# Kernel tuning notes

Measured on AMD Instinct MI355X. Metric: run time of the kernel, lower is better.

Reference implementation:

```python
import jax, jax.numpy as jnp
import numpy as np

N_EMBD = 768

def setup_inputs() -> dict:
    key = jax.random.key(0)
    k1, k2, k3, k4 = jax.random.split(key, 4)
    B, T, head_size = 16, 1024, 128
    x = jax.random.normal(k1, (B, T, N_EMBD), dtype=jnp.float32)
    # nn.Linear(in, out, bias=False): weight stored as (out, in); we store transposed (in, out)
    s = 1.0 / np.sqrt(N_EMBD)
    Wk = jax.random.uniform(k2, (N_EMBD, head_size), jnp.float32, -s, s)
    Wq = jax.random.uniform(k3, (N_EMBD, head_size), jnp.float32, -s, s)
    Wv = jax.random.uniform(k4, (N_EMBD, head_size), jnp.float32, -s, s)
    return {"x": x, "Wk": Wk, "Wq": Wq, "Wv": Wv}

def reference(x, Wk, Wq, Wv):
    B, T, C = x.shape  # C == n_embd == 768
    k = jnp.einsum('btc,ch->bth', x, Wk)
    q = jnp.einsum('btc,ch->bth', x, Wq)
    v = jnp.einsum('btc,ch->bth', x, Wv)
    # NOTE: original scales by C**-0.5 with C = n_embd (768), not head_size.
    wei = jnp.einsum('bth,bsh->bts', q, k) * (C ** -0.5)  # (B, T, T)
    causal = jnp.tril(jnp.ones((T, T), dtype=bool))
    wei = jnp.where(causal, wei, -jnp.inf)
    wei = jax.nn.softmax(wei, axis=-1)
    # dropout p=0.0 -> identity
    return jnp.einsum('bts,bsh->bth', wei, v)
```

## Files before the change

### kernel.cpp

```cpp
#include <hip/hip_runtime.h>
#include <math.h>

#define NTOK   16384
#define NEMBD  768
#define HDIM   128

typedef __attribute__((ext_vector_type(8)))  short short8;
typedef __attribute__((ext_vector_type(16))) float floatx16;

#define MFMA32(a,b,c) __builtin_amdgcn_mfma_f32_32x32x16_bf16(a,b,c,0,0,0)

__device__ __forceinline__ unsigned short f2bf(float f) {
    unsigned u = __float_as_uint(f);
    u += 0x7fff + ((u >> 16) & 1);
    return (unsigned short)(u >> 16);
}
__device__ __forceinline__ unsigned pack2(float a, float b) {
    unsigned r;
    asm("v_cvt_pk_bf16_f32 %0, %1, %2" : "=v"(r) : "v"(a), "v"(b));
    return r;
}
__device__ __forceinline__ unsigned pack2_trunc(float a, float b) {
    return __builtin_amdgcn_perm(__float_as_uint(b), __float_as_uint(a),
                                 0x07060302u);
}
__device__ __forceinline__ void gl_lds16(const void* gptr, void* lptr) {
    __builtin_amdgcn_global_load_lds(
        (const __attribute__((address_space(1))) unsigned int*)gptr,
        (__attribute__((address_space(3))) unsigned int*)lptr, 16, 0, 0);
}

__global__ __launch_bounds__(256) void prep_w(
    const float* __restrict__ Wk, const float* __restrict__ Wq,
    const float* __restrict__ Wv, unsigned short* __restrict__ wt)
{
    __shared__ float T[64 * 65];

    const int tid = threadIdx.x;
    const int bw  = blockIdx.x / 24;
    const int rem = blockIdx.x % 24;
    const int ct  = rem >> 1, dh = rem & 1;
    const int c0  = ct * 64, d0 = dh * 64;
    const float* W = (bw == 0) ? Wk : ((bw == 1) ? Wq : Wv);
    const float scale = (bw == 1)
        ? (0.03608439182435161f * 1.4426950408889634f) : 1.0f;

    #pragma unroll
    for (int pass = 0; pass < 4; ++pass) {
        int idx = pass * 256 + tid;
        int c  = idx >> 4;
        int d4 = idx & 15;
        float4 v = ((const float4*)W)[(size_t)(c0 + c) * 32 + dh * 16 + d4];
        v.x *= scale; v.y *= scale; v.z *= scale; v.w *= scale;
        T[(d4 * 4 + 0) * 65 + c] = v.x;
        T[(d4 * 4 + 1) * 65 + c] = v.y;
        T[(d4 * 4 + 2) * 65 + c] = v.z;
        T[(d4 * 4 + 3) * 65 + c] = v.w;
    }
    __syncthreads();

    #pragma unroll
    for (int pass = 0; pass < 2; ++pass) {
        int idx = pass * 256 + tid;
        int d  = idx >> 3;
        int c8 = idx & 7;
        const float* row = &T[d * 65 + c8 * 8];
        uint4 u = make_uint4(pack2(row[0], row[1]), pack2(row[2], row[3]),
                             pack2(row[4], row[5]), pack2(row[6], row[7]));
        *(uint4*)&wt[(size_t)bw * (HDIM * NEMBD) + (size_t)(d0 + d) * NEMBD
                     + c0 + c8 * 8] = u;
    }
}

__global__ __launch_bounds__(256) void qkv_fused(
    const float* __restrict__ x, const unsigned short* __restrict__ wt,
    unsigned short* __restrict__ kb, unsigned short* __restrict__ qb,
    unsigned short* __restrict__ vT)
{
    __shared__ __align__(16) char As[8192];
    __shared__ __align__(16) char Bs[24576];

    const int tid = threadIdx.x, w = tid >> 6, lane = tid & 63;
    const int l31 = lane & 31, h = lane >> 5;
    const int r8 = lane >> 3, c8 = lane & 7;
    const int wm = w >> 1, wn = w & 1;
    const int bid = blockIdx.x;
    const int b2  = ((bid & 7) << 6) | (bid >> 3);
    const int mtile = b2 >> 1, nh = b2 & 1;
    const int m0 = mtile * 64;
    const int nbase = nh * 192;
    const int arow = tid >> 2, ac = tid & 3;

    floatx16 acc[3];
    #pragma unroll
    for (int j = 0; j < 3; ++j)
        #pragma unroll
        for (int i = 0; i < 16; ++i) acc[j][i] = 0.f;

    const float* asrc = x + (size_t)(m0 + arow) * NEMBD + ac * 16;
    float4 a0 = ((const float4*)asrc)[0];
    float4 a1 = ((const float4*)asrc)[1];
    float4 a2 = ((const float4*)asrc)[2];
    float4 a3 = ((const float4*)asrc)[3];

    for (int it = 0; it < 12; ++it) {
        const int k0 = it * 64;
        __syncthreads();
        #pragma unroll
        for (int j = 0; j < 6; ++j) {
            int rowb = w * 48 + j * 8;
            int row  = rowb + r8;
            gl_lds16((const char*)wt + ((size_t)(nbase + row) * NEMBD + k0) * 2
                         + ((c8 ^ (row & 7)) * 16),
                     Bs + rowb * 128);
        }
        {
            uint4 u0 = make_uint4(pack2(a0.x, a0.y), pack2(a0.z, a0.w),
                                  pack2(a1.x, a1.y), pack2(a1.z, a1.w));
            uint4 u1 = make_uint4(pack2(a2.x, a2.y), pack2(a2.z, a2.w),
                                  pack2(a3.x, a3.y), pack2(a3.z, a3.w));
            int cA = 2 * ac, cB = 2 * ac + 1;
            *(uint4*)(As + arow * 128 + ((cA ^ (arow & 7)) * 16)) = u0;
            *(uint4*)(As + arow * 128 + ((cB ^ (arow & 7)) * 16)) = u1;
        }
        if (it < 11) {
            const float4* src = (const float4*)(asrc + (it + 1) * 64);
            a0 = src[0]; a1 = src[1]; a2 = src[2]; a3 = src[3];
        }
        __syncthreads();
        #pragma unroll
        for (int ks = 0; ks < 4; ++ks) {
            int ar = wm * 32 + l31;
            short8 af = *(const short8*)(As + ar * 128
                                         + (((2*ks + h) ^ (ar & 7)) * 16));
            #pragma unroll
            for (int j = 0; j < 3; ++j) {
                int br = wn * 96 + j * 32 + l31;
                short8 bf = *(const short8*)(Bs + br * 128
                                             + (((2*ks + h) ^ (br & 7)) * 16));
                acc[j] = MFMA32(af, bf, acc[j]);
            }
        }
    }

    const int tbase = m0 + wm * 32;
    #pragma unroll
    for (int j = 0; j < 3; ++j) {
        int n0 = nbase + wn * 96 + j * 32;
        if (n0 < 256) {
            unsigned short* outp = (n0 < 128) ? kb : qb;
            int d = (n0 & 127) + l31;
            #pragma unroll
            for (int r = 0; r < 16; ++r) {
                int t = tbase + (r & 3) + 8 * (r >> 2) + 4 * h;
                outp[(size_t)t * HDIM + d] = f2bf(acc[j][r]);
            }
        } else {
            int d = (n0 - 256) + l31, b = m0 >> 10, tloc = (m0 & 1023) + wm * 32;
            #pragma unroll
            for (int g = 0; g < 4; ++g) {
                int t = tloc + 8 * g + 4 * h;
                uint2 u = make_uint2(pack2(acc[j][4*g+0], acc[j][4*g+1]),
                                     pack2(acc[j][4*g+2], acc[j][4*g+3]));
                *(uint2*)((char*)vT + (((size_t)(b * HDIM + d)) * 1024 + t) * 2) = u;
            }
        }
    }
}

__global__ __launch_bounds__(256) void attn_mfma(
    const unsigned short* __restrict__ qb, const unsigned short* __restrict__ kb,
    const unsigned short* __restrict__ vT, float* __restrict__ out)
{
    __shared__ __align__(16) float Obuf[4 * 32 * 128];
    __shared__ float lred[128];

    const int tid = threadIdx.x, w = tid >> 6, lane = tid & 63;
    const int l31 = lane & 31, h = lane >> 5;
    const int u  = blockIdx.x & 255;
    const int b  = u & 15, p = u >> 4;
    const int qt = (blockIdx.x >> 8) ? (31 - p) : p;

    const char* kb_b = (const char*)kb + (size_t)b * (1024 * 256);
    const char* qb_b = (const char*)qb + (size_t)b * (1024 * 256);
    const char* vT_b = (const char*)vT + (size_t)b * (HDIM * 2048);

    short8 qf[8];
    {
        const char* qrow = qb_b + (size_t)(qt * 32 + l31) * 256 + h * 16;
        #pragma unroll
        for (int ks = 0; ks < 8; ++ks)
            qf[ks] = *(const short8*)(qrow + ks * 32);
    }

    floatx16 o[4];
    #pragma unroll
    for (int nt = 0; nt < 4; ++nt)
        #pragma unroll
        for (int i = 0; i < 16; ++i) o[nt][i] = 0.f;
    float l_r = 0.f;

    short8 kf[8];
    if (w <= qt) {
        const char* krow = kb_b + (size_t)(w * 32 + l31) * 256 + h * 16;
        #pragma unroll
        for (int ks = 0; ks < 8; ++ks)
            kf[ks] = *(const short8*)(krow + ks * 32);
    }

    for (int st = w; st <= qt; st += 4) {
        short8 vf[8];
        {
            const char* vrow0 = vT_b + (size_t)l31 * 2048 + (size_t)st * 64 + h * 16;
            #pragma unroll
            for (int nt = 0; nt < 4; ++nt) {
                const char* vr = vrow0 + (size_t)nt * (32 * 2048);
                vf[nt * 2 + 0] = *(const short8*)(vr + 0);
                vf[nt * 2 + 1] = *(const short8*)(vr + 32);
            }
        }
        floatx16 s;
        #pragma unroll
        for (int i = 0; i < 16; ++i) s[i] = 0.f;
        __builtin_amdgcn_s_setprio(1);
        #pragma unroll
        for (int ks = 0; ks < 8; ++ks) s = MFMA32(kf[ks], qf[ks], s);
        __builtin_amdgcn_s_setprio(0);

        if (st + 4 <= qt) {
            const char* krow = kb_b + (size_t)((st + 4) * 32 + l31) * 256 + h * 16;
            #pragma unroll
            for (int ks = 0; ks < 8; ++ks)
                kf[ks] = *(const short8*)(krow + ks * 32);
        }

        if (st == qt) {
            #pragma unroll
            for (int r = 0; r < 16; ++r) {
                int key = (r & 3) + 8 * (r >> 2) + 4 * h;
                if (key > l31) s[r] = -1e30f;
            }
        }
        float p16[16];
        float ps0 = 0.f, ps1 = 0.f, ps2 = 0.f, ps3 = 0.f;
        #pragma unroll
        for (int r = 0; r < 4; ++r) {
            p16[4*r+0] = __builtin_amdgcn_exp2f(s[4*r+0]);
            p16[4*r+1] = __builtin_amdgcn_exp2f(s[4*r+1]);
            p16[4*r+2] = __builtin_amdgcn_exp2f(s[4*r+2]);
            p16[4*r+3] = __builtin_amdgcn_exp2f(s[4*r+3]);
            ps0 += p16[4*r+0]; ps1 += p16[4*r+1];
            ps2 += p16[4*r+2]; ps3 += p16[4*r+3];
        }
        l_r += (ps0 + ps1) + (ps2 + ps3);

        unsigned own[8];
        #pragma unroll
        for (int i = 0; i < 8; ++i) own[i] = pack2_trunc(p16[2*i], p16[2*i+1]);
        asm("v_permlane32_swap_b32 %0, %1" : "+v"(own[0]), "+v"(own[2]));
        asm("v_permlane32_swap_b32 %0, %1" : "+v"(own[1]), "+v"(own[3]));
        asm("v_permlane32_swap_b32 %0, %1" : "+v"(own[4]), "+v"(own[6]));
        asm("v_permlane32_swap_b32 %0, %1" : "+v"(own[5]), "+v"(own[7]));
        short8 pf[2];
        {
            union { short8 v; unsigned uu[4]; } f0, f1;
            f0.uu[0]=own[0]; f0.uu[1]=own[1]; f0.uu[2]=own[2]; f0.uu[3]=own[3];
            f1.uu[0]=own[4]; f1.uu[1]=own[5]; f1.uu[2]=own[6]; f1.uu[3]=own[7];
            pf[0] = f0.v; pf[1] = f1.v;
        }
        __builtin_amdgcn_s_setprio(1);
        #pragma unroll
        for (int nt = 0; nt < 4; ++nt) {
            o[nt] = MFMA32(vf[nt * 2 + 0], pf[0], o[nt]);
            o[nt] = MFMA32(vf[nt * 2 + 1], pf[1], o[nt]);
        }
        __builtin_amdgcn_s_setprio(0);
    }

    l_r += __shfl_xor(l_r, 32, 64);
    if (lane < 32) lred[w * 32 + l31] = l_r;
    {
        float* mybuf = &Obuf[w * 4096];
        #pragma unroll
        for (int nt = 0; nt < 4; ++nt) {
            #pragma unroll
            for (int g = 0; g < 4; ++g) {
                int chunk = nt * 8 + 2 * g + h;
                int slot  = (chunk & 24) | ((chunk & 7) ^ (l31 & 7));
                *((float4*)&mybuf[l31 * 128] + slot) =
                    make_float4(o[nt][4*g+0], o[nt][4*g+1],
                                o[nt][4*g+2], o[nt][4*g+3]);
            }
        }
    }
    __syncthreads();
    {
        int q  = tid >> 3;
        int cb = (tid & 7) * 4;
        float inv = 1.f / (lred[q] + lred[32 + q] + lred[64 + q] + lred[96 + q]);
        #pragma unroll
        for (int cc = 0; cc < 4; ++cc) {
            int chunk = cb + cc;
            int slot  = (chunk & 24) | ((chunk & 7) ^ (q & 7));
            float4 v0 = *((float4*)&Obuf[0 * 4096 + q * 128] + slot);
            float4 v1 = *((float4*)&Obuf[1 * 4096 + q * 128] + slot);
            float4 v2 = *((float4*)&Obuf[2 * 4096 + q * 128] + slot);
            float4 v3 = *((float4*)&Obuf[3 * 4096 + q * 128] + slot);
            float4 v = make_float4((v0.x + v1.x + v2.x + v3.x) * inv,
                                   (v0.y + v1.y + v2.y + v3.y) * inv,
                                   (v0.z + v1.z + v2.z + v3.z) * inv,
                                   (v0.w + v1.w + v2.w + v3.w) * inv);
            *(float4*)&out[((size_t)(b * 1024 + qt * 32 + q)) * HDIM + chunk * 4] = v;
        }
    }
}

extern "C" void kernel_launch(void* const* d_in, const int* in_sizes, int n_in,
                              void* d_out, int out_size, void* d_ws, size_t ws_size,
                              hipStream_t stream)
{
    const float* x  = (const float*)d_in[0];
    const float* Wk = (const float*)d_in[1];
    const float* Wq = (const float*)d_in[2];
    const float* Wv = (const float*)d_in[3];
    float* outp = (float*)d_out;

    char* ws = (char*)d_ws;
    unsigned short* wt = (unsigned short*)(ws);
    unsigned short* kb = (unsigned short*)(ws + 589824);
    unsigned short* qb = (unsigned short*)(ws + 4784128);
    unsigned short* vT = (unsigned short*)(ws + 8978432);

    prep_w<<<72, 256, 0, stream>>>(Wk, Wq, Wv, wt);
    qkv_fused<<<512, 256, 0, stream>>>(x, wt, kb, qb, vT);
    attn_mfma<<<512, 256, 0, stream>>>(qb, kb, vT, outp);
}
```

Measured before the change: 131.8 us.

## Double-buffer LDS tiles in QKV projection GEMM to overlap loads with MFMA

Converts the QKV projection's shared-memory A and B tiles into ping-pong buffers. The next k-slice's weight tile is issued by async global-to-LDS loads and the activation tile is converted and stored while the current slice runs through MFMA, which cuts one barrier per iteration. It also drops the block-index swizzle in favor of a linear mapping, and replaces the hardware packed bf16 convert with a software round-and-shift. Doubling LDS to about 64KB per block may reduce occupancy, and the software convert costs extra ALU instructions.

```diff
diff --git a/kernel.cpp b/kernel.cpp
--- a/kernel.cpp
+++ b/kernel.cpp
@@ -16,9 +16,7 @@
     return (unsigned short)(u >> 16);
 }
 __device__ __forceinline__ unsigned pack2(float a, float b) {
-    unsigned r;
-    asm("v_cvt_pk_bf16_f32 %0, %1, %2" : "=v"(r) : "v"(a), "v"(b));
-    return r;
+    return (unsigned)f2bf(a) | ((unsigned)f2bf(b) << 16);
 }
 __device__ __forceinline__ unsigned pack2_trunc(float a, float b) {
     return __builtin_amdgcn_perm(__float_as_uint(b), __float_as_uint(a),
@@ -77,16 +75,14 @@
     unsigned short* __restrict__ kb, unsigned short* __restrict__ qb,
     unsigned short* __restrict__ vT)
 {
-    __shared__ __align__(16) char As[8192];
-    __shared__ __align__(16) char Bs[24576];
+    __shared__ __align__(16) char As[2][8192];
+    __shared__ __align__(16) char Bs[2][24576];
 
     const int tid = threadIdx.x, w = tid >> 6, lane = tid & 63;
     const int l31 = lane & 31, h = lane >> 5;
     const int r8 = lane >> 3, c8 = lane & 7;
     const int wm = w >> 1, wn = w & 1;
-    const int bid = blockIdx.x;
-    const int b2  = ((bid & 7) << 6) | (bid >> 3);
-    const int mtile = b2 >> 1, nh = b2 & 1;
+    const int mtile = blockIdx.x >> 1, nh = blockIdx.x & 1;
     const int m0 = mtile * 64;
     const int nbase = nh * 192;
     const int arow = tid >> 2, ac = tid & 3;
@@ -98,49 +94,82 @@
         for (int i = 0; i < 16; ++i) acc[j][i] = 0.f;
 
     const float* asrc = x + (size_t)(m0 + arow) * NEMBD + ac * 16;
+
+    #pragma unroll
+    for (int j = 0; j < 6; ++j) {
+        int rowb = w * 48 + j * 8;
+        int row  = rowb + r8;
+        gl_lds16((const char*)wt + ((size_t)(nbase + row) * NEMBD) * 2
+                     + ((c8 ^ (row & 7)) * 16),
+                 Bs[0] + rowb * 128);
+    }
     float4 a0 = ((const float4*)asrc)[0];
     float4 a1 = ((const float4*)asrc)[1];
     float4 a2 = ((const float4*)asrc)[2];
     float4 a3 = ((const float4*)asrc)[3];
-
+    {
+        uint4 u0 = make_uint4(pack2(a0.x, a0.y), pack2(a0.z, a0.w),
+                              pack2(a1.x, a1.y), pack2(a1.z, a1.w));
+        uint4 u1 = make_uint4(pack2(a2.x, a2.y), pack2(a2.z, a2.w),
+                              pack2(a3.x, a3.y), pack2(a3.z, a3.w));
+        int cA = 2 * ac, cB = 2 * ac + 1;
+        *(uint4*)(As[0] + arow * 128 + ((cA ^ (arow & 7)) * 16)) = u0;
+        *(uint4*)(As[0] + arow * 128 + ((cB ^ (arow & 7)) * 16)) = u1;
+    }
+    {
+        const float4* src = (const float4*)(asrc + 64);
+        a0 = src[0]; a1 = src[1]; a2 = src[2]; a3 = src[3];
+    }
+    __syncthreads();
+
+    #pragma unroll
     for (int it = 0; it < 12; ++it) {
-        const int k0 = it * 64;
-        __syncthreads();
-        #pragma unroll
-        for (int j = 0; j < 6; ++j) {
-            int rowb = w * 48 + j * 8;
-            int row  = rowb + r8;
-            gl_lds16((const char*)wt + ((size_t)(nbase + row) * NEMBD + k0) * 2
-                         + ((c8 ^ (row & 7)) * 16),
-                     Bs + rowb * 128);
-        }
-        {
+        char* Acur = As[it & 1];
+        char* Bcur = Bs[it & 1];
+        char* Anxt = As[(it & 1) ^ 1];
+        char* Bnxt = Bs[(it & 1) ^ 1];
+
+        if (it < 11) {
+            const int k0n = (it + 1) * 64;
+            #pragma unroll
+            for (int j = 0; j < 6; ++j) {
+                int rowb = w * 48 + j * 8;
+                int row  = rowb + r8;
+                gl_lds16((const char*)wt
+                             + ((size_t)(nbase + row) * NEMBD + k0n) * 2
+                             + ((c8 ^ (row & 7)) * 16),
+                         Bnxt + rowb * 128);
+            }
+        }
+
+        #pragma unroll
+        for (int ks = 0; ks < 4; ++ks) {
+            int ar = wm * 32 + l31;
+            short8 af = *(const short8*)(Acur + ar * 128
+                                         + (((2*ks + h) ^ (ar & 7)) * 16));
+            #pragma unroll
+            for (int j = 0; j < 3; ++j) {
+                int br = wn * 96 + j * 32 + l31;
+                short8 bf = *(const short8*)(Bcur + br * 128
+                                             + (((2*ks + h) ^ (br & 7)) * 16));
+                acc[j] = MFMA32(af, bf, acc[j]);
+            }
+        }
+
+        if (it < 11) {
             uint4 u0 = make_uint4(pack2(a0.x, a0.y), pack2(a0.z, a0.w),
                                   pack2(a1.x, a1.y), pack2(a1.z, a1.w));
             uint4 u1 = make_uint4(pack2(a2.x, a2.y), pack2(a2.z, a2.w),
                                   pack2(a3.x, a3.y), pack2(a3.z, a3.w));
             int cA = 2 * ac, cB = 2 * ac + 1;
-            *(uint4*)(As + arow * 128 + ((cA ^ (arow & 7)) * 16)) = u0;
-            *(uint4*)(As + arow * 128 + ((cB ^ (arow & 7)) * 16)) = u1;
-        }
-        if (it < 11) {
-            const float4* src = (const float4*)(asrc + (it + 1) * 64);
-            a0 = src[0]; a1 = src[1]; a2 = src[2]; a3 = src[3];
+            *(uint4*)(Anxt + arow * 128 + ((cA ^ (arow & 7)) * 16)) = u0;
+            *(uint4*)(Anxt + arow * 128 + ((cB ^ (arow & 7)) * 16)) = u1;
+            if (it < 10) {
+                const float4* src = (const float4*)(asrc + (it + 2) * 64);
+                a0 = src[0]; a1 = src[1]; a2 = src[2]; a3 = src[3];
+            }
         }
         __syncthreads();
-        #pragma unroll
-        for (int ks = 0; ks < 4; ++ks) {
-            int ar = wm * 32 + l31;
-            short8 af = *(const short8*)(As + ar * 128
-                                         + (((2*ks + h) ^ (ar & 7)) * 16));
-            #pragma unroll
-            for (int j = 0; j < 3; ++j) {
-                int br = wn * 96 + j * 32 + l31;
-                short8 bf = *(const short8*)(Bs + br * 128
-                                             + (((2*ks + h) ^ (br & 7)) * 16));
-                acc[j] = MFMA32(af, bf, acc[j]);
-            }
-        }
     }
 
     const int tbase = m0 + wm * 32;
```

New measurement: 125.3 us. -5.0%, faster.
